# Kernel optimization log

Hardware: AMD Instinct MI355X
Metric: run time of the kernel (lower is better)

## Reference

```python
import jax, jax.numpy as jnp
import numpy as np

EPS = 1e-06

def setup_inputs() -> dict:
    key = jax.random.key(0)
    k1, k2, k3, k4 = jax.random.split(key, 4)
    N, E, D = 100000, 1600000, 128
    feat = jax.random.normal(k1, (N, D), dtype=jnp.float32)
    src = jax.random.randint(k2, (E,), 0, N, dtype=jnp.int32)
    dst = jax.random.randint(k3, (E,), 0, N, dtype=jnp.int32)
    W = jax.random.normal(k4, (D, D), dtype=jnp.float32) * 0.05
    b = jnp.zeros((D,), dtype=jnp.float32)
    a2 = jnp.ones((D,), dtype=jnp.float32)
    b2 = jnp.zeros((D,), dtype=jnp.float32)
    return {"feat": feat, "src": src, "dst": dst, "W": W, "b": b, "a2": a2, "b2": b2}

def reference(feat, src, dst, W, b, a2, b2):
    N, D = feat.shape
    # LayerNorm (torch std is unbiased, eps added to std, not var)
    mean = jnp.mean(feat, axis=-1, keepdims=True)
    std = jnp.std(feat, axis=-1, keepdims=True, ddof=1)
    h = a2 * (feat - mean) / (std + EPS) + b2
    # DGL GraphConv, norm='both': D_out^{-1/2} gather-sum D_in^{-1/2}, then W, b, relu
    ones = jnp.ones(src.shape[0], dtype=feat.dtype)
    out_deg = jax.ops.segment_sum(ones, src, num_segments=N)
    in_deg = jax.ops.segment_sum(ones, dst, num_segments=N)
    norm_out = jax.lax.rsqrt(jnp.maximum(out_deg, 1.0))[:, None]
    norm_in = jax.lax.rsqrt(jnp.maximum(in_deg, 1.0))[:, None]
    h = h * norm_out
    # in_feats == out_feats -> DGL multiplies weight first
    h = h @ W
    agg = jax.ops.segment_sum(h[src], dst, num_segments=N)  # [N, D]
    rst = agg * norm_in + b
    rst = jax.nn.relu(rst)
    # residual (Identity since in_feats == out_feats); dropout is identity at eval
    return rst + feat
```

## Files before the change

kernel.cpp:

```cpp
#include <hip/hip_runtime.h>

#define D 128
#define BSH 6
#define BN 64
#define NBUK_MAX 2048
#define NBLK 256
#define SRT_CAP 2048
#define NW_LDS 25600

typedef __bf16 bf16x8 __attribute__((ext_vector_type(8)));
typedef float  f32x4  __attribute__((ext_vector_type(4)));

__device__ __forceinline__ unsigned short f2bf(float f) {
    unsigned u = __float_as_uint(f);
    unsigned r = (u + 0x7FFF + ((u >> 16) & 1)) >> 16;
    return (unsigned short)r;
}
__device__ __forceinline__ float bf2f(unsigned short s) {
    return __uint_as_float(((unsigned)s) << 16);
}

__global__ __launch_bounds__(1024) void count_kernel(const int* __restrict__ src,
        const int* __restrict__ dst, const float* __restrict__ W,
        unsigned short* __restrict__ Wp, int* __restrict__ hist,
        unsigned* __restrict__ partial, int E, int nbuk, int chunk, int NW) {
    __shared__ unsigned ph[NW_LDS];
    __shared__ int hb[NBUK_MAX];
    int t = threadIdx.x;

    if (blockIdx.x < 16) {
        int idx = blockIdx.x * 1024 + t;
        int k = idx >> 7;
        int c = idx & 127;
        Wp[c * D + (k ^ ((c & 7) << 3))] = f2bf(W[idx]);
    }

    for (int i = t; i < NW_LDS; i += 1024) ph[i] = 0;
    for (int i = t; i < nbuk; i += 1024) hb[i] = 0;
    __syncthreads();
    int lo = blockIdx.x * chunk;
    int hi = min(E, lo + chunk);
    for (int e = lo + t; e < hi; e += 1024) {
        int s = src[e], d = dst[e];
        atomicAdd(&ph[s >> 2], 1u << ((s & 3) * 8));
        atomicAdd(&hb[d >> BSH], 1);
    }
    __syncthreads();
    int* hrow = hist + (size_t)blockIdx.x * nbuk;
    for (int i = t; i < nbuk; i += 1024) hrow[i] = hb[i];
    unsigned* prow = partial + (size_t)blockIdx.x * NW;
    for (int i = t; i < NW; i += 1024) prow[i] = ph[i];
}

__global__ __launch_bounds__(1024) void rh_kernel(const unsigned* __restrict__ partial,
        unsigned* __restrict__ podeg, int NW, int nrb,
        int* __restrict__ hist, int* __restrict__ colsum, int nbuk) {
    if ((int)blockIdx.x < nrb) {
        __shared__ unsigned acc[16][64];
        int t = threadIdx.x;
        int wl = t & 63, bg = t >> 6;
        int w = blockIdx.x * 64 + wl;
        unsigned s = 0;
        if (w < NW) {
            for (int b = bg; b < NBLK; b += 16) s += partial[(size_t)b * NW + w];
        }
        acc[bg][wl] = s;
        __syncthreads();
        if (bg == 0 && w < NW) {
            unsigned tot = 0;
            #pragma unroll
            for (int g = 0; g < 16; ++g) tot += acc[g][wl];
            podeg[w] = tot;
        }
    } else {
        int buk = blockIdx.x - nrb;
        int l = threadIdx.x;
        if (l < 64 && buk < nbuk) {
            int v[4]; int s = 0;
            #pragma unroll
            for (int i = 0; i < 4; ++i) {
                v[i] = hist[(size_t)(l * 4 + i) * nbuk + buk];
                s += v[i];
            }
            int x = s;
            #pragma unroll
            for (int m = 1; m < 64; m <<= 1) {
                int y = __shfl_up(x, m);
                if (l >= m) x += y;
            }
            int base = x - s;
            #pragma unroll
            for (int i = 0; i < 4; ++i) {
                int tmp = v[i];
                hist[(size_t)(l * 4 + i) * nbuk + buk] = base;
                base += tmp;
            }
            if (l == 63) colsum[buk] = x;
        }
    }
}

__global__ __launch_bounds__(1024) void bscan_kernel(const int* __restrict__ colsum,
        int* __restrict__ base, int nbuk, int E) {
    __shared__ int s[1024];
    int t = threadIdx.x;
    int i0 = 2 * t, i1 = 2 * t + 1;
    int a = (i0 < nbuk) ? colsum[i0] : 0;
    int c = (i1 < nbuk) ? colsum[i1] : 0;
    int p = a + c;
    s[t] = p;
    __syncthreads();
    #pragma unroll
    for (int off = 1; off < 1024; off <<= 1) {
        int x = (t >= off) ? s[t - off] : 0;
        __syncthreads();
        s[t] += x;
        __syncthreads();
    }
    int ex = s[t] - p;
    if (i0 < nbuk) base[i0] = ex;
    if (i1 < nbuk) base[i1] = ex + a;
    if (t == 0) base[nbuk] = E;
}

__global__ __launch_bounds__(512) void mid_kernel(const int* __restrict__ src,
        const int* __restrict__ dst, const int* __restrict__ hist,
        const int* __restrict__ base, unsigned* __restrict__ pairs,
        int E, int nbuk, int chunk,
        const float* __restrict__ feat, const unsigned short* __restrict__ Wp,
        const float* __restrict__ a2, const float* __restrict__ b2,
        const unsigned* __restrict__ podeg, unsigned short* __restrict__ hw, int N) {
    __shared__ union U {
        int cur[NBUK_MAX];
        struct {
            unsigned short hs[128 * D];
            unsigned short Wt[D * D];
        } g;
        __device__ U() {}
    } u;

    const int t = threadIdx.x;

    if ((int)blockIdx.x < NBLK) {
        const int* hrow = hist + (size_t)blockIdx.x * nbuk;
        for (int i = t; i < nbuk; i += 512) u.cur[i] = base[i] + hrow[i];
        __syncthreads();
        int lo = blockIdx.x * chunk;
        int hi = min(E, lo + chunk);
        for (int e = lo + t; e < hi; e += 512) {
            int d = dst[e];
            int pos = atomicAdd(&u.cur[d >> BSH], 1);
            pairs[pos] = ((unsigned)(d & (BN - 1)) << 24) | (unsigned)src[e];
        }
        return;
    }

    const int rbase = (blockIdx.x - NBLK) * 128;

    {
        const uint4* Wp4 = (const uint4*)Wp;
        uint4* Wl4 = (uint4*)u.g.Wt;
        #pragma unroll
        for (int i = 0; i < 4; ++i) Wl4[i * 512 + t] = Wp4[i * 512 + t];
    }

    {
        const int r = t >> 2;
        const int sub = t & 3;
        const int grow = rbase + r;
        const bool valid = grow < N;

        float4 v[8];
        float sum = 0.f, sumsq = 0.f;
        if (valid) {
            const float4* fr = (const float4*)(feat + (size_t)grow * D + sub * 32);
            #pragma unroll
            for (int i = 0; i < 8; ++i) {
                v[i] = fr[i];
                sum   += v[i].x + v[i].y + v[i].z + v[i].w;
                sumsq += v[i].x * v[i].x + v[i].y * v[i].y + v[i].z * v[i].z + v[i].w * v[i].w;
            }
        }
        sum   += __shfl_xor(sum, 1);   sumsq += __shfl_xor(sumsq, 1);
        sum   += __shfl_xor(sum, 2);   sumsq += __shfl_xor(sumsq, 2);

        if (valid) {
            float mean = sum * (1.f / 128.f);
            float var  = fmaxf((sumsq - 128.f * mean * mean) * (1.f / 127.f), 0.f);
            float inv  = 1.f / (sqrtf(var) + 1e-6f);
            int   od   = (podeg[grow >> 2] >> ((grow & 3) * 8)) & 0xFF;
            float norm = rsqrtf(fmaxf((float)od, 1.f));
            float sa   = inv * norm;
            #pragma unroll
            for (int i = 0; i < 8; ++i) {
                int c0 = sub * 32 + i * 4;
                float4 av = *(const float4*)&a2[c0];
                float4 bv = *(const float4*)&b2[c0];
                ushort4 o;
                o.x = f2bf(av.x * (v[i].x - mean) * sa + bv.x * norm);
                o.y = f2bf(av.y * (v[i].y - mean) * sa + bv.y * norm);
                o.z = f2bf(av.z * (v[i].z - mean) * sa + bv.z * norm);
                o.w = f2bf(av.w * (v[i].w - mean) * sa + bv.w * norm);
                *(ushort4*)&u.g.hs[r * D + (c0 ^ ((r & 7) << 3))] = o;
            }
        } else {
            ushort4 z = make_ushort4(0, 0, 0, 0);
            #pragma unroll
            for (int i = 0; i < 8; ++i) {
                int c0 = sub * 32 + i * 4;
                *(ushort4*)&u.g.hs[r * D + (c0 ^ ((r & 7) << 3))] = z;
            }
        }
    }
    __syncthreads();

    {
        const int w = t >> 6;
        const int l = t & 63;
        const int lrow = l & 15;
        const int kg = l >> 4;
        const int arow = w * 16 + lrow;

        bf16x8 a[4];
        #pragma unroll
        for (int kt = 0; kt < 4; ++kt) {
            int col = kt * 32 + kg * 8;
            a[kt] = *reinterpret_cast<const bf16x8*>(&u.g.hs[arow * D + (col ^ ((arow & 7) << 3))]);
        }

        f32x4 acc[8];
        #pragma unroll
        for (int ct = 0; ct < 8; ++ct) acc[ct] = (f32x4){0.f, 0.f, 0.f, 0.f};

        #pragma unroll
        for (int ct = 0; ct < 8; ++ct) {
            int brow = ct * 16 + lrow;
            #pragma unroll
            for (int kt = 0; kt < 4; ++kt) {
                int col = kt * 32 + kg * 8;
                bf16x8 bfr = *reinterpret_cast<const bf16x8*>(&u.g.Wt[brow * D + (col ^ ((brow & 7) << 3))]);
                acc[ct] = __builtin_amdgcn_mfma_f32_16x16x32_bf16(a[kt], bfr, acc[ct], 0, 0, 0);
            }
        }

        #pragma unroll
        for (int ct = 0; ct < 8; ++ct) {
            #pragma unroll
            for (int p = 0; p < 4; ++p) {
                int gr = rbase + w * 16 + kg * 4 + p;
                if (gr < N) hw[(size_t)gr * D + ct * 16 + lrow] = f2bf(acc[ct][p]);
            }
        }
    }
}

__global__ __launch_bounds__(512) void gather_kernel(const unsigned* __restrict__ pairs,
        const int* __restrict__ bukbase, const unsigned short* __restrict__ hw,
        const float* __restrict__ feat, const float* __restrict__ bias,
        float* __restrict__ out, int N) {
    __shared__ unsigned srt[SRT_CAP];
    __shared__ int cnt[BN];
    __shared__ int ofs[BN + 1];

    int t = threadIdx.x;
    int buk = blockIdx.x;
    int beg = bukbase[buk];
    int ne = bukbase[buk + 1] - beg;
    if (ne > SRT_CAP) ne = SRT_CAP;

    if (t < BN) cnt[t] = 0;
    __syncthreads();

    for (int i = t; i < ne; i += 512)
        atomicAdd(&cnt[pairs[beg + i] >> 24], 1);
    __syncthreads();

    if (t < BN) {
        int c = cnt[t];
        int x = c;
        #pragma unroll
        for (int m = 1; m < BN; m <<= 1) {
            int y = __shfl_up(x, m);
            if (t >= m) x += y;
        }
        ofs[t] = x - c;
        if (t == BN - 1) ofs[BN] = x;
        cnt[t] = x - c;
    }
    __syncthreads();

    for (int i = t; i < ne; i += 512) {
        unsigned p = pairs[beg + i];
        int pos = atomicAdd(&cnt[p >> 24], 1);
        srt[pos] = p & 0xFFFFFFu;
    }
    __syncthreads();

    int wv = t >> 6;
    int lane = t & 63;
    int half = lane >> 5;
    int l32 = lane & 31;
    int co = l32 * 4;

    for (int nl = wv; nl < BN; nl += 8) {
        int n = (buk << BSH) + nl;
        if (n >= N) break;
        int s0 = ofs[nl], s1 = ofs[nl + 1];
        int deg = s1 - s0;

        float a0 = 0.f, a1 = 0.f, a2v = 0.f, a3 = 0.f;
        int e = s0 + half;
        for (; e + 6 < s1; e += 8) {
            int x0 = srt[e], x1 = srt[e + 2], x2 = srt[e + 4], x3 = srt[e + 6];
            ushort4 q0 = *(const ushort4*)&hw[(size_t)x0 * D + co];
            ushort4 q1 = *(const ushort4*)&hw[(size_t)x1 * D + co];
            ushort4 q2 = *(const ushort4*)&hw[(size_t)x2 * D + co];
            ushort4 q3 = *(const ushort4*)&hw[(size_t)x3 * D + co];
            a0  += bf2f(q0.x) + bf2f(q1.x) + bf2f(q2.x) + bf2f(q3.x);
            a1  += bf2f(q0.y) + bf2f(q1.y) + bf2f(q2.y) + bf2f(q3.y);
            a2v += bf2f(q0.z) + bf2f(q1.z) + bf2f(q2.z) + bf2f(q3.z);
            a3  += bf2f(q0.w) + bf2f(q1.w) + bf2f(q2.w) + bf2f(q3.w);
        }
        for (; e < s1; e += 2) {
            int x0 = srt[e];
            ushort4 q0 = *(const ushort4*)&hw[(size_t)x0 * D + co];
            a0  += bf2f(q0.x);
            a1  += bf2f(q0.y);
            a2v += bf2f(q0.z);
            a3  += bf2f(q0.w);
        }

        a0  += __shfl_xor(a0, 32);
        a1  += __shfl_xor(a1, 32);
        a2v += __shfl_xor(a2v, 32);
        a3  += __shfl_xor(a3, 32);

        if (half == 0) {
            float ni = rsqrtf(fmaxf((float)deg, 1.f));
            float4 bb = *(const float4*)&bias[co];
            float4 f  = *(const float4*)&feat[(size_t)n * D + co];
            float4 o;
            o.x = fmaxf(fmaf(a0,  ni, bb.x), 0.f) + f.x;
            o.y = fmaxf(fmaf(a1,  ni, bb.y), 0.f) + f.y;
            o.z = fmaxf(fmaf(a2v, ni, bb.z), 0.f) + f.z;
            o.w = fmaxf(fmaf(a3,  ni, bb.w), 0.f) + f.w;
            *(float4*)&out[(size_t)n * D + co] = o;
        }
    }
}

extern "C" void kernel_launch(void* const* d_in, const int* in_sizes, int n_in,
                              void* d_out, int out_size, void* d_ws, size_t ws_size,
                              hipStream_t stream) {
    const float* feat = (const float*)d_in[0];
    const int*   src  = (const int*)d_in[1];
    const int*   dst  = (const int*)d_in[2];
    const float* W    = (const float*)d_in[3];
    const float* b    = (const float*)d_in[4];
    const float* a2   = (const float*)d_in[5];
    const float* b2   = (const float*)d_in[6];

    const int N = in_sizes[0] / D;
    const int E = in_sizes[1];
    const int NW = (N + 3) / 4;
    const int nbuk = (N + BN - 1) >> BSH;
    const int chunk = (E + NBLK - 1) / NBLK;
    const int nrb = (NW + 63) / 64;
    const int nln = (N + 127) / 128;

    float* out = (float*)d_out;

    unsigned short* hw = (unsigned short*)d_ws;
    unsigned* podeg = (unsigned*)(hw + (size_t)N * D);
    int* hist    = (int*)(podeg + NW);
    int* colsum  = hist + (size_t)NBLK * NBUK_MAX;
    int* bukbase = colsum + NBUK_MAX;
    unsigned short* Wp = (unsigned short*)(bukbase + (NBUK_MAX + 1));
    unsigned* pairs = (unsigned*)(Wp + D * D);
    unsigned* partial = pairs + E;

    count_kernel<<<NBLK, 1024, 0, stream>>>(src, dst, W, Wp, hist, partial, E, nbuk, chunk, NW);
    rh_kernel<<<nrb + nbuk, 1024, 0, stream>>>(partial, podeg, NW, nrb, hist, colsum, nbuk);
    bscan_kernel<<<1, 1024, 0, stream>>>(colsum, bukbase, nbuk, E);
    mid_kernel<<<NBLK + nln, 512, 0, stream>>>(src, dst, hist, bukbase, pairs, E, nbuk, chunk,
                                               feat, Wp, a2, b2, podeg, hw, N);
    gather_kernel<<<nbuk, 512, 0, stream>>>(pairs, bukbase, hw, feat, b, out, N);
}
```

Before: 148.5 us.

## Split gather feature columns across XCD halves to shrink per-XCD L2 working set

The gather kernel now launches two blocks per destination bucket, each handling 64 of the 128 feature columns. Blocks are mapped so that XCDs 0-3 get the low column half and XCDs 4-7 the high half, assuming round-robin block-to-XCD dispatch. The intent is that each XCD's L2 caches only half of every bf16 hw row, improving hit rates on the random source gathers. In exchange, every bucket's pairs are read and sorted twice in LDS, loads are narrowed to ushort2, and blocks drop to 256 threads.

```diff
diff --git a/kernel.cpp b/kernel.cpp
--- a/kernel.cpp
+++ b/kernel.cpp
@@ -254,16 +254,21 @@
     }
 }
 
-__global__ __launch_bounds__(512) void gather_kernel(const unsigned* __restrict__ pairs,
+__global__ __launch_bounds__(256) void gather_kernel(const unsigned* __restrict__ pairs,
         const int* __restrict__ bukbase, const unsigned short* __restrict__ hw,
         const float* __restrict__ feat, const float* __restrict__ bias,
-        float* __restrict__ out, int N) {
+        float* __restrict__ out, int N, int nbuk) {
     __shared__ unsigned srt[SRT_CAP];
     __shared__ int cnt[BN];
     __shared__ int ofs[BN + 1];
 
     int t = threadIdx.x;
-    int buk = blockIdx.x;
+    int b = blockIdx.x;
+    int xcd = b & 7;
+    int half = xcd >> 2;
+    int buk = (b >> 3) * 4 + (xcd & 3);
+    if (buk >= nbuk) return;
+
     int beg = bukbase[buk];
     int ne = bukbase[buk + 1] - beg;
     if (ne > SRT_CAP) ne = SRT_CAP;
@@ -271,7 +276,7 @@
     if (t < BN) cnt[t] = 0;
     __syncthreads();
 
-    for (int i = t; i < ne; i += 512)
+    for (int i = t; i < ne; i += 256)
         atomicAdd(&cnt[pairs[beg + i] >> 24], 1);
     __syncthreads();
 
@@ -289,7 +294,7 @@
     }
     __syncthreads();
 
-    for (int i = t; i < ne; i += 512) {
+    for (int i = t; i < ne; i += 256) {
         unsigned p = pairs[beg + i];
         int pos = atomicAdd(&cnt[p >> 24], 1);
         srt[pos] = p & 0xFFFFFFu;
@@ -298,53 +303,45 @@
 
     int wv = t >> 6;
     int lane = t & 63;
-    int half = lane >> 5;
+    int ehalf = lane >> 5;
     int l32 = lane & 31;
-    int co = l32 * 4;
-
-    for (int nl = wv; nl < BN; nl += 8) {
+    int co = half * 64 + l32 * 2;
+
+    for (int nl = wv; nl < BN; nl += 4) {
         int n = (buk << BSH) + nl;
         if (n >= N) break;
         int s0 = ofs[nl], s1 = ofs[nl + 1];
         int deg = s1 - s0;
 
-        float a0 = 0.f, a1 = 0.f, a2v = 0.f, a3 = 0.f;
-        int e = s0 + half;
+        float a0 = 0.f, a1 = 0.f;
+        int e = s0 + ehalf;
         for (; e + 6 < s1; e += 8) {
             int x0 = srt[e], x1 = srt[e + 2], x2 = srt[e + 4], x3 = srt[e + 6];
-            ushort4 q0 = *(const ushort4*)&hw[(size_t)x0 * D + co];
-            ushort4 q1 = *(const ushort4*)&hw[(size_t)x1 * D + co];
-            ushort4 q2 = *(const ushort4*)&hw[(size_t)x2 * D + co];
-            ushort4 q3 = *(const ushort4*)&hw[(size_t)x3 * D + co];
-            a0  += bf2f(q0.x) + bf2f(q1.x) + bf2f(q2.x) + bf2f(q3.x);
-            a1  += bf2f(q0.y) + bf2f(q1.y) + bf2f(q2.y) + bf2f(q3.y);
-            a2v += bf2f(q0.z) + bf2f(q1.z) + bf2f(q2.z) + bf2f(q3.z);
-            a3  += bf2f(q0.w) + bf2f(q1.w) + bf2f(q2.w) + bf2f(q3.w);
+            ushort2 q0 = *(const ushort2*)&hw[(size_t)x0 * D + co];
+            ushort2 q1 = *(const ushort2*)&hw[(size_t)x1 * D + co];
+            ushort2 q2 = *(const ushort2*)&hw[(size_t)x2 * D + co];
+            ushort2 q3 = *(const ushort2*)&hw[(size_t)x3 * D + co];
+            a0 += bf2f(q0.x) + bf2f(q1.x) + bf2f(q2.x) + bf2f(q3.x);
+            a1 += bf2f(q0.y) + bf2f(q1.y) + bf2f(q2.y) + bf2f(q3.y);
         }
         for (; e < s1; e += 2) {
             int x0 = srt[e];
-            ushort4 q0 = *(const ushort4*)&hw[(size_t)x0 * D + co];
-            a0  += bf2f(q0.x);
-            a1  += bf2f(q0.y);
-            a2v += bf2f(q0.z);
-            a3  += bf2f(q0.w);
-        }
-
-        a0  += __shfl_xor(a0, 32);
-        a1  += __shfl_xor(a1, 32);
-        a2v += __shfl_xor(a2v, 32);
-        a3  += __shfl_xor(a3, 32);
-
-        if (half == 0) {
+            ushort2 q0 = *(const ushort2*)&hw[(size_t)x0 * D + co];
+            a0 += bf2f(q0.x);
+            a1 += bf2f(q0.y);
+        }
+
+        a0 += __shfl_xor(a0, 32);
+        a1 += __shfl_xor(a1, 32);
+
+        if (ehalf == 0) {
             float ni = rsqrtf(fmaxf((float)deg, 1.f));
-            float4 bb = *(const float4*)&bias[co];
-            float4 f  = *(const float4*)&feat[(size_t)n * D + co];
-            float4 o;
-            o.x = fmaxf(fmaf(a0,  ni, bb.x), 0.f) + f.x;
-            o.y = fmaxf(fmaf(a1,  ni, bb.y), 0.f) + f.y;
-            o.z = fmaxf(fmaf(a2v, ni, bb.z), 0.f) + f.z;
-            o.w = fmaxf(fmaf(a3,  ni, bb.w), 0.f) + f.w;
-            *(float4*)&out[(size_t)n * D + co] = o;
+            float2 bb = *(const float2*)&bias[co];
+            float2 f  = *(const float2*)&feat[(size_t)n * D + co];
+            float2 o;
+            o.x = fmaxf(fmaf(a0, ni, bb.x), 0.f) + f.x;
+            o.y = fmaxf(fmaf(a1, ni, bb.y), 0.f) + f.y;
+            *(float2*)&out[(size_t)n * D + co] = o;
         }
     }
 }
@@ -367,6 +364,7 @@
     const int chunk = (E + NBLK - 1) / NBLK;
     const int nrb = (NW + 63) / 64;
     const int nln = (N + 127) / 128;
+    const int G = (nbuk + 3) / 4;
 
     float* out = (float*)d_out;
 
@@ -384,5 +382,5 @@
     bscan_kernel<<<1, 1024, 0, stream>>>(colsum, bukbase, nbuk, E);
     mid_kernel<<<NBLK + nln, 512, 0, stream>>>(src, dst, hist, bukbase, pairs, E, nbuk, chunk,
                                                feat, Wp, a2, b2, podeg, hw, N);
-    gather_kernel<<<nbuk, 512, 0, stream>>>(pairs, bukbase, hw, feat, b, out, N);
-}
+    gather_kernel<<<8 * G, 256, 0, stream>>>(pairs, bukbase, hw, feat, b, out, N, nbuk);
+}
```

New measurement: 158.8 us. 1.07x slower.
